# Optimization experiments

Hardware: AMD Instinct MI355X
Metric: run time of the kernel (lower is better)

## Reference

```python
import jax, jax.numpy as jnp
import numpy as np

B, D, K = 4, 128, 512   # batch, node_embedding_dim, num_nodes
ALPHA = 0.2             # LeakyReLU negative slope


def setup_inputs() -> dict:
    key = jax.random.key(0)
    k1, k2, k3, k4 = jax.random.split(key, 4)
    x = jax.random.normal(k1, (B, D, K), dtype=jnp.float32)
    # nn.Linear(2D -> D): store weight as (2D, D) for right-multiplication
    lin_w = jax.random.normal(k2, (2 * D, D), dtype=jnp.float32) * (1.0 / np.sqrt(2 * D))
    lin_b = jax.random.normal(k3, (D,), dtype=jnp.float32) * 0.01
    # attention vector a: (D,) (xavier-uniform in torch; scale-equivalent normal here)
    a = jax.random.normal(k4, (D,), dtype=jnp.float32) * (1.414 * np.sqrt(2.0 / (D + 1)))
    bias_mat = jnp.zeros((K, K), dtype=jnp.float32)  # init zeros per module
    return {"x": x, "lin_w": lin_w, "lin_b": lin_b, "a": a, "bias_mat": bias_mat}


def reference(x, lin_w, lin_b, a, bias_mat):
    # x: (B, D, K) -> transpose to (B, K, D); GATv2 path, residual = identity
    xt = jnp.swapaxes(x, 1, 2)                      # (B, K, D)
    d = xt.shape[-1]
    # lin(concat(v_i, v_j)) == v_i @ W1 + v_j @ W2 + b  (exact split; avoids (B,K,K,2D) concat)
    W1, W2 = lin_w[:d], lin_w[d:]
    left = xt @ W1 + lin_b                          # (B, K, D) -- v_i part (repeating block)
    right = xt @ W2                                 # (B, K, D) -- v_j part (alternating block)
    pre = left[:, :, None, :] + right[:, None, :, :]  # (B, K, K, D)
    h = jnp.where(pre > 0, pre, ALPHA * pre)        # LeakyReLU
    e = jnp.einsum('bijd,d->bij', h, a) + bias_mat  # (B, K, K)
    attn = jax.nn.softmax(e, axis=2)                # softmax over j (dropout p=0)
    agg = jnp.einsum('bij,bjd->bid', attn, xt)      # (B, K, D)
    out = jax.nn.sigmoid(agg) + xt                  # sigmoid + identity residual
    return jnp.swapaxes(out, 1, 2)                  # (B, D, K)
```

## Files before the change

### kernel.cpp

```cpp
#include <hip/hip_runtime.h>

#define B 4
#define D 128
#define K 512
#define TI 4

typedef __fp16 h2v __attribute__((ext_vector_type(2)));

__device__ __forceinline__ unsigned pkrtz(float a, float b) {
  h2v h = __builtin_amdgcn_cvt_pkrtz(a, b);
  union { h2v h; unsigned u; } c; c.h = h; return c.u;
}
__device__ __forceinline__ h2v u2h(unsigned u) {
  union { unsigned u; h2v h; } c; c.u = u; return c.h;
}
__device__ __forceinline__ float fdot2f(h2v a, h2v b, float c) {
#if __has_builtin(__builtin_amdgcn_fdot2)
  return __builtin_amdgcn_fdot2(a, b, c, false);
#else
  return c + (float)a.x * (float)b.x + (float)a.y * (float)b.y;
#endif
}
__device__ __forceinline__ h2v relu2(h2v a) {
#if __has_builtin(__builtin_elementwise_max)
  const h2v z = {(__fp16)0.f, (__fp16)0.f};
  return __builtin_elementwise_max(a, z);
#else
  h2v r;
  r.x = (float)a.x > 0.f ? a.x : (__fp16)0.f;
  r.y = (float)a.y > 0.f ? a.y : (__fp16)0.f;
  return r;
#endif
}

__global__ __launch_bounds__(256) void gat_lr16(
    const float* __restrict__ x, const float* __restrict__ lin_w,
    const float* __restrict__ lin_b, const float* __restrict__ a,
    unsigned* __restrict__ LhT, unsigned* __restrict__ RhT,
    unsigned* __restrict__ XhT) {
  const int j0 = blockIdx.x * 64;
  const int E0 = blockIdx.y * 16;
  const int b = blockIdx.z;
  const int t = threadIdx.x;
  __shared__ float sx[D][64];
  __shared__ float sw1[D][16];
  __shared__ float sw2[D][16];
#pragma unroll
  for (int r = 0; r < 8; ++r) {
    const int fid = t + 256 * r;
    const int row = fid >> 4, c4 = fid & 15;
    *(float4*)&sx[row][4 * c4] =
        *(const float4*)&x[((size_t)b * D + row) * K + j0 + 4 * c4];
  }
#pragma unroll
  for (int r = 0; r < 8; ++r) {
    const int idx = t + 256 * r;
    const int row = idx >> 4, e = idx & 15;
    sw1[row][e] = lin_w[(size_t)row * D + E0 + e];
    sw2[row][e] = lin_w[(size_t)(D + row) * D + E0 + e];
  }
  __syncthreads();
  if (E0 == 0) {
#pragma unroll
    for (int r = 0; r < 16; ++r) {
      const int idx = t + 256 * r;
      const int row = idx >> 5, jc = idx & 31;
      XhT[((size_t)b * D + row) * (K / 2) + (j0 >> 1) + jc] =
          pkrtz(sx[row][2 * jc], sx[row][2 * jc + 1]);
    }
  }
  const int j = t & 63, g = t >> 6;
  float accL[4] = {0.f, 0.f, 0.f, 0.f}, accR[4] = {0.f, 0.f, 0.f, 0.f};
#pragma unroll 8
  for (int c = 0; c < D; ++c) {
    const float xv = sx[c][j];
    const float4 w1 = *(const float4*)&sw1[c][4 * g];
    const float4 w2 = *(const float4*)&sw2[c][4 * g];
    accL[0] = fmaf(xv, w1.x, accL[0]);
    accL[1] = fmaf(xv, w1.y, accL[1]);
    accL[2] = fmaf(xv, w1.z, accL[2]);
    accL[3] = fmaf(xv, w1.w, accL[3]);
    accR[0] = fmaf(xv, w2.x, accR[0]);
    accR[1] = fmaf(xv, w2.y, accR[1]);
    accR[2] = fmaf(xv, w2.z, accR[2]);
    accR[3] = fmaf(xv, w2.w, accR[3]);
  }
  const int e0 = E0 + 4 * g;
#pragma unroll
  for (int u = 0; u < 2; ++u) {
    const int ea = e0 + 2 * u, eb = ea + 1;
    const float uea = 0.8f * fabsf(a[ea]), ueb = 0.8f * fabsf(a[eb]);
    const float La = uea * (accL[2 * u] + lin_b[ea]);
    const float Lb = ueb * (accL[2 * u + 1] + lin_b[eb]);
    const float Ra = uea * accR[2 * u];
    const float Rb = ueb * accR[2 * u + 1];
    const size_t dp = (size_t)(ea >> 1);
    LhT[((size_t)b * (D / 2) + dp) * K + j0 + j] = pkrtz(La, Lb);
    RhT[((size_t)b * (D / 2) + dp) * K + j0 + j] = pkrtz(Ra, Rb);
  }
}

__global__ __launch_bounds__(256) void gat_attn16(
    const float* __restrict__ x, const float* __restrict__ a,
    const float* __restrict__ bias, const unsigned* __restrict__ LhT,
    const unsigned* __restrict__ RhT, const unsigned* __restrict__ XhT,
    float* __restrict__ out) {
  const int i0 = blockIdx.x * TI;
  const int b = blockIdx.y;
  const int t = threadIdx.x;
  __shared__ float sxt[D][TI];
  __shared__ unsigned slh[D / 2][TI];
  __shared__ unsigned ssg[D / 2];
  __shared__ float sSL[TI];
  __shared__ float seT[TI][K];
  __shared__ unsigned sattn16[TI][K / 2];

  {
    int idx = t;
    sxt[idx >> 2][idx & 3] = x[((size_t)b * D + (idx >> 2)) * K + i0 + (idx & 3)];
    idx = t + 256;
    sxt[idx >> 2][idx & 3] = x[((size_t)b * D + (idx >> 2)) * K + i0 + (idx & 3)];
    const int dp = t >> 2, ii = t & 3;
    slh[dp][ii] = LhT[((size_t)b * (D / 2) + dp) * K + i0 + ii];
    if (t < D / 2) {
      const float s0 = (a[2 * t] >= 0.f) ? 1.f : -1.f;
      const float s1 = (a[2 * t + 1] >= 0.f) ? 1.f : -1.f;
      ssg[t] = pkrtz(s0, s1);
    }
  }
  __syncthreads();
  {
    const int ii = t >> 6, dp = t & 63;
    float v = fdot2f(u2h(ssg[dp]), u2h(slh[dp][ii]), 0.f);
#pragma unroll
    for (int off = 32; off > 0; off >>= 1) v += __shfl_xor(v, off, 64);
    if ((t & 63) == 0) sSL[ii] = v;
  }
  __syncthreads();

  {
    const unsigned* rc = RhT + (size_t)b * (D / 2) * K;
    float accA[4] = {0.f, 0.f, 0.f, 0.f}, accB[4] = {0.f, 0.f, 0.f, 0.f};
    float srA = 0.f, srB = 0.f;
#pragma unroll 4
    for (int dp = 0; dp < D / 2; ++dp) {
      const uint2 rr = *(const uint2*)&rc[(size_t)dp * K + 2 * t];
      const uint4 lh4 = *(const uint4*)&slh[dp][0];
      const h2v s2 = u2h(ssg[dp]);
      const h2v rva = u2h(rr.x), rvb = u2h(rr.y);
      srA = fdot2f(s2, rva, srA);
      srB = fdot2f(s2, rvb, srB);
      h2v l;
      l = u2h(lh4.x);
      accA[0] = fdot2f(s2, relu2(l + rva), accA[0]);
      accB[0] = fdot2f(s2, relu2(l + rvb), accB[0]);
      l = u2h(lh4.y);
      accA[1] = fdot2f(s2, relu2(l + rva), accA[1]);
      accB[1] = fdot2f(s2, relu2(l + rvb), accB[1]);
      l = u2h(lh4.z);
      accA[2] = fdot2f(s2, relu2(l + rva), accA[2]);
      accB[2] = fdot2f(s2, relu2(l + rvb), accB[2]);
      l = u2h(lh4.w);
      accA[3] = fdot2f(s2, relu2(l + rva), accA[3]);
      accB[3] = fdot2f(s2, relu2(l + rvb), accB[3]);
    }
#pragma unroll
    for (int ii = 0; ii < TI; ++ii) {
      const float2 bv = *(const float2*)&bias[(size_t)(i0 + ii) * K + 2 * t];
      float2 ev;
      ev.x = accA[ii] + 0.25f * (sSL[ii] + srA) + bv.x;
      ev.y = accB[ii] + 0.25f * (sSL[ii] + srB) + bv.y;
      *(float2*)&seT[ii][2 * t] = ev;
    }
  }
  __syncthreads();

  {
    const int w = t >> 6, lane = t & 63;
    float2 v[4];
    float m = -1e30f;
#pragma unroll
    for (int q = 0; q < 4; ++q) {
      v[q] = *(const float2*)&seT[w][2 * lane + 128 * q];
      m = fmaxf(m, fmaxf(v[q].x, v[q].y));
    }
#pragma unroll
    for (int off = 32; off > 0; off >>= 1) m = fmaxf(m, __shfl_xor(m, off, 64));
    float s = 0.f;
#pragma unroll
    for (int q = 0; q < 4; ++q) {
      v[q].x = __expf(v[q].x - m);
      v[q].y = __expf(v[q].y - m);
      s += v[q].x + v[q].y;
    }
#pragma unroll
    for (int off = 32; off > 0; off >>= 1) s += __shfl_xor(s, off, 64);
    const float inv = 1.f / s;
#pragma unroll
    for (int q = 0; q < 4; ++q)
      sattn16[w][lane + 64 * q] = pkrtz(v[q].x * inv, v[q].y * inv);
  }
  __syncthreads();

  {
    const int l = t & 63, w = t >> 6;
    const int iL = l & 3, cg = l >> 2;
    const unsigned* xh = XhT + (size_t)b * D * (K / 2);
    for (int r = 0; r < 32; ++r) {
      const int d = w * 32 + r;
      float acc = 0.f;
#pragma unroll
      for (int q = 0; q < 4; ++q) {
        const int c8 = cg + 16 * q;
        const uint4 xp = *(const uint4*)&xh[(size_t)d * (K / 2) + 4 * c8];
        const uint4 ap = *(const uint4*)&sattn16[iL][4 * c8];
        acc = fdot2f(u2h(ap.x), u2h(xp.x), acc);
        acc = fdot2f(u2h(ap.y), u2h(xp.y), acc);
        acc = fdot2f(u2h(ap.z), u2h(xp.z), acc);
        acc = fdot2f(u2h(ap.w), u2h(xp.w), acc);
      }
#pragma unroll
      for (int off = 4; off < 64; off <<= 1) acc += __shfl_xor(acc, off, 64);
      if (cg == 0) {
        const float sg = 1.f / (1.f + __expf(-acc));
        out[((size_t)b * D + d) * K + i0 + iL] = sg + sxt[d][iL];
      }
    }
  }
}

#define ALPHA 0.2f
__global__ __launch_bounds__(512) void gat_fused(
    const float* __restrict__ x, const float* __restrict__ lin_w,
    const float* __restrict__ lin_b, const float* __restrict__ a,
    const float* __restrict__ bias, float* __restrict__ out) {
  const int i = blockIdx.x, b = blockIdx.y, t = threadIdx.x;
  __shared__ float sxi[D], sLi[D], sa[D];
  __shared__ float lpart[4 * D];
  __shared__ float xtT[D * 64];
  __shared__ float epars[8 * 64];
  __shared__ float se[K];
  __shared__ float sattn[K], spart[K];
  __shared__ float sred[8];

  if (t < D) {
    sxi[t] = x[((size_t)b * D + t) * K + i];
    sa[t] = a[t];
  }
  __syncthreads();
  {
    const int c = t & (D - 1), q = t >> 7;
    float acc = 0.f;
    const float* W1 = lin_w + c;
#pragma unroll 8
    for (int d = q * 32; d < q * 32 + 32; ++d)
      acc = fmaf(sxi[d], W1[(size_t)d * D], acc);
    lpart[q * D + c] = acc;
  }
  __syncthreads();
  if (t < D)
    sLi[t] = lin_b[t] + lpart[t] + lpart[D + t] + lpart[2 * D + t] +
             lpart[3 * D + t];
  __syncthreads();

  for (int jt = 0; jt < K / 64; ++jt) {
    const int j0 = jt * 64;
    for (int idx = t; idx < D * 64; idx += 512)
      xtT[idx] = x[((size_t)b * D + (idx >> 6)) * K + j0 + (idx & 63)];
    __syncthreads();
    const int jj = t & 63, g = t >> 6, dp0 = g * 16;
    float accv[16];
#pragma unroll
    for (int v = 0; v < 16; ++v) accv[v] = 0.f;
    for (int dc = 0; dc < D; dc += 16) {
      float xv[16];
#pragma unroll
      for (int u = 0; u < 16; ++u) xv[u] = xtT[(dc + u) * 64 + jj];
#pragma unroll
      for (int u = 0; u < 16; ++u) {
        const float* W2r = lin_w + (size_t)(D + dc + u) * D + dp0;
#pragma unroll
        for (int v = 0; v < 16; ++v) accv[v] = fmaf(xv[u], W2r[v], accv[v]);
      }
    }
    float ep = 0.f;
#pragma unroll
    for (int v = 0; v < 16; ++v) {
      const float pre = sLi[dp0 + v] + accv[v];
      ep = fmaf(sa[dp0 + v], pre > 0.f ? pre : ALPHA * pre, ep);
    }
    epars[g * 64 + jj] = ep;
    __syncthreads();
    if (t < 64) {
      float esum = bias[(size_t)i * K + j0 + t];
#pragma unroll
      for (int g2 = 0; g2 < 8; ++g2) esum += epars[g2 * 64 + t];
      se[j0 + t] = esum;
    }
    __syncthreads();
  }

  float e = se[t];
  float m = e;
#pragma unroll
  for (int off = 32; off > 0; off >>= 1) m = fmaxf(m, __shfl_xor(m, off, 64));
  if ((t & 63) == 0) sred[t >> 6] = m;
  __syncthreads();
  m = sred[0];
#pragma unroll
  for (int w = 1; w < 8; ++w) m = fmaxf(m, sred[w]);
  const float ev = __expf(e - m);
  float s = ev;
#pragma unroll
  for (int off = 32; off > 0; off >>= 1) s += __shfl_xor(s, off, 64);
  __syncthreads();
  if ((t & 63) == 0) sred[t >> 6] = s;
  __syncthreads();
  s = 0.f;
#pragma unroll
  for (int w = 0; w < 8; ++w) s += sred[w];
  sattn[t] = ev * (1.f / s);
  __syncthreads();

  const int d = t >> 2, c = t & 3;
  const float4* X4 = (const float4*)(x + ((size_t)b * D + d) * K);
  const float4* A4 = (const float4*)sattn;
  float p = 0.f;
#pragma unroll 4
  for (int q = 0; q < K / 16; ++q) {
    const int idx = c + 4 * q;
    float4 xv = X4[idx], av = A4[idx];
    p = fmaf(av.x, xv.x, p);
    p = fmaf(av.y, xv.y, p);
    p = fmaf(av.z, xv.z, p);
    p = fmaf(av.w, xv.w, p);
  }
  spart[t] = p;
  __syncthreads();
  if (t < D) {
    const float agg =
        spart[4 * t] + spart[4 * t + 1] + spart[4 * t + 2] + spart[4 * t + 3];
    const float sg = 1.f / (1.f + __expf(-agg));
    out[((size_t)b * D + t) * K + i] = sg + sxi[t];
  }
}

extern "C" void kernel_launch(void* const* d_in, const int* in_sizes, int n_in,
                              void* d_out, int out_size, void* d_ws,
                              size_t ws_size, hipStream_t stream) {
  const float* x = (const float*)d_in[0];
  const float* lin_w = (const float*)d_in[1];
  const float* lin_b = (const float*)d_in[2];
  const float* a = (const float*)d_in[3];
  const float* bias = (const float*)d_in[4];
  float* out = (float*)d_out;

  const size_t half_words = (size_t)B * (D / 2) * K;
  const size_t xh_words = (size_t)B * D * (K / 2);
  const size_t need = (2 * half_words + xh_words) * sizeof(unsigned);
  if (ws_size >= need && d_ws != nullptr) {
    unsigned* LhT = (unsigned*)d_ws;
    unsigned* RhT = LhT + half_words;
    unsigned* XhT = RhT + half_words;
    gat_lr16<<<dim3(K / 64, D / 16, B), 256, 0, stream>>>(x, lin_w, lin_b, a,
                                                          LhT, RhT, XhT);
    gat_attn16<<<dim3(K / TI, B), 256, 0, stream>>>(x, a, bias, LhT, RhT, XhT,
                                                    out);
  } else {
    gat_fused<<<dim3(K, B), 512, 0, stream>>>(x, lin_w, lin_b, a, bias, out);
  }
}
```

Measured before the change: 96.47 us.

## Register-block attention rows in aggregation and spread fp16 transpose writes across blocks

The aggregation stage now loads the 4 attention rows into registers once and reuses each loaded fp16 x vector across all 4 query rows. Each lane accumulates 4 outputs, reduced over 16 lanes instead of 64, which cuts redundant global/LDS loads and shuffle work per output. Separately, writing the fp16 transposed x copy is split across blocks by blockIdx.y, so every block writes two rows instead of only the E0==0 blocks writing sixteen. This assumes the grid's y dimension covers exactly eight slices. The register blocking raises register pressure.

```diff
diff --git a/kernel.cpp b/kernel.cpp
--- a/kernel.cpp
+++ b/kernel.cpp
@@ -60,9 +60,10 @@
     sw2[row][e] = lin_w[(size_t)(D + row) * D + E0 + e];
   }
   __syncthreads();
-  if (E0 == 0) {
-#pragma unroll
-    for (int r = 0; r < 16; ++r) {
+  {
+    const int ry = blockIdx.y * 2;
+#pragma unroll
+    for (int r = ry; r < ry + 2; ++r) {
       const int idx = t + 256 * r;
       const int row = idx >> 5, jc = idx & 31;
       XhT[((size_t)b * D + row) * (K / 2) + (j0 >> 1) + jc] =
@@ -203,27 +204,43 @@
   __syncthreads();
 
   {
-    const int l = t & 63, w = t >> 6;
-    const int iL = l & 3, cg = l >> 2;
+    const int jr = t & 15, dg = t >> 4;
+    uint4 ar[4][4];
+#pragma unroll
+    for (int i = 0; i < 4; ++i)
+#pragma unroll
+      for (int q = 0; q < 4; ++q)
+        ar[i][q] = *(const uint4*)&sattn16[i][4 * (jr + 16 * q)];
     const unsigned* xh = XhT + (size_t)b * D * (K / 2);
-    for (int r = 0; r < 32; ++r) {
-      const int d = w * 32 + r;
-      float acc = 0.f;
+#pragma unroll 2
+    for (int r = 0; r < 8; ++r) {
+      const int d = dg * 8 + r;
+      float acc[4] = {0.f, 0.f, 0.f, 0.f};
 #pragma unroll
       for (int q = 0; q < 4; ++q) {
-        const int c8 = cg + 16 * q;
-        const uint4 xp = *(const uint4*)&xh[(size_t)d * (K / 2) + 4 * c8];
-        const uint4 ap = *(const uint4*)&sattn16[iL][4 * c8];
-        acc = fdot2f(u2h(ap.x), u2h(xp.x), acc);
-        acc = fdot2f(u2h(ap.y), u2h(xp.y), acc);
-        acc = fdot2f(u2h(ap.z), u2h(xp.z), acc);
-        acc = fdot2f(u2h(ap.w), u2h(xp.w), acc);
+        const uint4 xp =
+            *(const uint4*)&xh[(size_t)d * (K / 2) + 4 * (jr + 16 * q)];
+#pragma unroll
+        for (int i = 0; i < 4; ++i) {
+          acc[i] = fdot2f(u2h(ar[i][q].x), u2h(xp.x), acc[i]);
+          acc[i] = fdot2f(u2h(ar[i][q].y), u2h(xp.y), acc[i]);
+          acc[i] = fdot2f(u2h(ar[i][q].z), u2h(xp.z), acc[i]);
+          acc[i] = fdot2f(u2h(ar[i][q].w), u2h(xp.w), acc[i]);
+        }
       }
 #pragma unroll
-      for (int off = 4; off < 64; off <<= 1) acc += __shfl_xor(acc, off, 64);
-      if (cg == 0) {
-        const float sg = 1.f / (1.f + __expf(-acc));
-        out[((size_t)b * D + d) * K + i0 + iL] = sg + sxt[d][iL];
+      for (int i = 0; i < 4; ++i) {
+        acc[i] += __shfl_xor(acc[i], 1, 64);
+        acc[i] += __shfl_xor(acc[i], 2, 64);
+        acc[i] += __shfl_xor(acc[i], 4, 64);
+        acc[i] += __shfl_xor(acc[i], 8, 64);
+      }
+      if (jr == 0) {
+#pragma unroll
+        for (int i = 0; i < 4; ++i) {
+          const float sg = 1.f / (1.f + __expf(-acc[i]));
+          out[((size_t)b * D + d) * K + i0 + i] = sg + sxt[d][i];
+        }
       }
     }
   }
```

Result: faster. 89.34 us (-7.4%).
